# Kernel optimization log

Measured on AMD Instinct MI355X. Metric: run time of the kernel, lower is better.

## Reference

```python
import jax, jax.numpy as jnp
import numpy as np

B, NP, NL, CIN, COUT, MID = 2048, 8, 4, 256, 256, 64


def setup_inputs() -> dict:
    key = jax.random.key(0)
    ks = jax.random.split(key, 16)
    s = 0.01  # small init scale (code uses xavier_normal with tiny gain)
    inp = {
        "x": jax.random.normal(ks[0], (B, CIN), jnp.float32),
        "h": jax.random.normal(ks[1], (B, NP), jnp.float32),
        "index": jnp.zeros((NL,), jnp.float32).at[0].set(1.0),  # one-hot layer index
        # target Linear params
        "target_w": jax.random.normal(ks[2], (COUT, CIN), jnp.float32) * (1.0 / np.sqrt(CIN)),
        "target_b": jax.random.normal(ks[3], (COUT,), jnp.float32) * 0.01,
        # embedder weight branch
        "fcwp_w": jax.random.normal(ks[4], (MID * CIN, NP), jnp.float32) * s,
        "fcwp_b": jnp.zeros((MID * CIN,), jnp.float32),
        "fcwi_w": jax.random.normal(ks[5], (MID * CIN, NL), jnp.float32) * s,
        "fcwi_b": jnp.zeros((MID * CIN,), jnp.float32),
        "fcwe_w": jax.random.normal(ks[6], (COUT, MID), jnp.float32) * s,
        "fcwe_b": jnp.zeros((COUT,), jnp.float32),
        # embedder bias branch
        "fcbp_w": jax.random.normal(ks[7], (COUT, NP), jnp.float32) * s,
        "fcbp_b": jnp.zeros((COUT,), jnp.float32),
        "fcbi_w": jax.random.normal(ks[8], (COUT, NL), jnp.float32) * s,
        "fcbi_b": jnp.zeros((COUT,), jnp.float32),
    }
    return inp


def reference(x, h, index, target_w, target_b,
              fcwp_w, fcwp_b, fcwi_w, fcwi_b, fcwe_w, fcwe_b,
              fcbp_w, fcbp_b, fcbi_w, fcbi_b):
    # --- embedder: per-sample weight modulation ---
    # w_flat: (B, mid*cin)
    w_flat = h @ fcwp_w.T + fcwp_b + (index @ fcwi_w.T + fcwi_b)
    w = w_flat.reshape(B, CIN, MID)                      # (B, cin, mid)
    w = jnp.einsum('bim,om->boi', w, fcwe_w) + fcwe_b[None, :, None]  # swapaxes folded in -> (B, out, cin)
    # bias modulation: (B, out)
    b = h @ fcbp_w.T + fcbp_b + (index @ fcbi_w.T + fcbi_b)
    # --- per-sample linear (grouped conv2d == batched GEMM) ---
    weights = target_w[None] + w                         # (B, out, cin)
    y = jnp.einsum('bi,boi->bo', x, weights)             # batched matvec
    y = y + target_b[None, :] + b
    return y
```

## Files before the change

### kernel.cpp

```cpp
#include <hip/hip_runtime.h>


#define B_TOT 2048
#define NP    8
#define CIN   256
#define COUT  256
#define MID   64
#define K2    352
#define LDG   576
#define LDAS  136
#define LDA2S 360
#define LDB2S 360

typedef short  short8  __attribute__((ext_vector_type(8)));
typedef float  floatx4 __attribute__((ext_vector_type(4)));

__device__ __forceinline__ unsigned short f2bf(float f) {
    union { float f; unsigned u; } v; v.f = f;
    unsigned r = v.u + 0x7FFFu + ((v.u >> 16) & 1u);
    return (unsigned short)(r >> 16);
}
__device__ __forceinline__ float bf2f(unsigned short u) {
    union { unsigned u; float f; } v; v.u = ((unsigned)u) << 16;
    return v.f;
}

__global__ __launch_bounds__(256) void setup_bb(
    const float* __restrict__ index,
    const float* __restrict__ fcwp_w, const float* __restrict__ fcwp_b,
    const float* __restrict__ fcwi_w, const float* __restrict__ fcwi_b,
    unsigned short* __restrict__ Bb)
{
    __shared__ unsigned short Lt[64][68];
    const int blk = blockIdx.x, tid = threadIdx.x;

    if (blk < 32) {
        const int i0 = (blk >> 3) * 64, n0 = (blk & 7) * 64;
        const int r = tid >> 4, c4 = (tid & 15) * 4;
        #pragma unroll
        for (int k = 0; k < 4; ++k) {
            int ii = r + k * 16;
            float4 v = *(const float4*)(fcwp_w + (size_t)(i0 + ii) * 512 + n0 + c4);
            Lt[c4 + 0][ii] = f2bf(v.x); Lt[c4 + 1][ii] = f2bf(v.y);
            Lt[c4 + 2][ii] = f2bf(v.z); Lt[c4 + 3][ii] = f2bf(v.w);
        }
        __syncthreads();
        const int nn = tid >> 2, ic0 = (tid & 3) * 16;
        #pragma unroll
        for (int k = 0; k < 4; ++k) {
            int ic = ic0 + k * 4;
            ushort4 o4;
            o4.x = Lt[nn][ic]; o4.y = Lt[nn][ic + 1];
            o4.z = Lt[nn][ic + 2]; o4.w = Lt[nn][ic + 3];
            *(ushort4*)&Bb[(size_t)(n0 + nn) * CIN + i0 + ic] = o4;
        }
    } else {
        const int i0 = (blk - 32) * 64;
        const float x0 = index[0], x1 = index[1], x2 = index[2], x3 = index[3];
        const int r = tid >> 4, c4 = (tid & 15) * 4;
        #pragma unroll
        for (int k = 0; k < 4; ++k) {
            int ii = r + k * 16;
            int e = (i0 + ii) * 64 + c4;
            float4 pb = *(const float4*)(fcwp_b + e);
            float4 ib = *(const float4*)(fcwi_b + e);
            float pbv[4] = {pb.x, pb.y, pb.z, pb.w};
            float ibv[4] = {ib.x, ib.y, ib.z, ib.w};
            #pragma unroll
            for (int j = 0; j < 4; ++j) {
                float4 wv = *(const float4*)(fcwi_w + (size_t)(e + j) * 4);
                Lt[c4 + j][ii] = f2bf(pbv[j] + ibv[j]
                    + x0 * wv.x + x1 * wv.y + x2 * wv.z + x3 * wv.w);
            }
        }
        __syncthreads();
        const int mm = tid >> 2, ic0 = (tid & 3) * 16;
        #pragma unroll
        for (int k = 0; k < 4; ++k) {
            int ic = ic0 + k * 4;
            ushort4 o4;
            o4.x = Lt[mm][ic]; o4.y = Lt[mm][ic + 1];
            o4.z = Lt[mm][ic + 2]; o4.w = Lt[mm][ic + 3];
            *(ushort4*)&Bb[(size_t)(512 + mm) * CIN + i0 + ic] = o4;
        }
    }
}

__global__ __launch_bounds__(256) void gemm1_kernel(
    const float* __restrict__ x,
    const unsigned short* __restrict__ Bb,
    const float* __restrict__ index,
    const float* __restrict__ target_w, const float* __restrict__ target_b,
    const float* __restrict__ fcwe_w, const float* __restrict__ fcwe_b,
    const float* __restrict__ fcbp_w, const float* __restrict__ fcbp_b,
    const float* __restrict__ fcbi_w, const float* __restrict__ fcbi_b,
    unsigned short* __restrict__ B2,
    unsigned short* __restrict__ G)
{
    __shared__ unsigned short As[64 * LDAS];
    __shared__ unsigned short Bs[64 * LDAS];
    const int blk = blockIdx.x, tid = threadIdx.x;

    if (blk < 288) {
        const int lane = tid & 63, w = tid >> 6;
        const int col = lane & 15, quad = lane >> 4;
        const int mb = (blk & 31) * 64, nb = (blk >> 5) * 64;

        floatx4 acc[4] = {floatx4{0,0,0,0}, floatx4{0,0,0,0},
                          floatx4{0,0,0,0}, floatx4{0,0,0,0}};

        for (int kh = 0; kh < 2; ++kh) {
            const int k0 = kh * 128;
            __syncthreads();
            #pragma unroll
            for (int it = 0; it < 8; ++it) {
                int idx = it * 256 + tid;
                int r = idx >> 5, c = (idx & 31) * 4;
                float4 v = *(const float4*)(x + (size_t)(mb + r) * CIN + k0 + c);
                ushort4 o4;
                o4.x = f2bf(v.x); o4.y = f2bf(v.y); o4.z = f2bf(v.z); o4.w = f2bf(v.w);
                *(ushort4*)&As[r * LDAS + c] = o4;
            }
            #pragma unroll
            for (int it = 0; it < 4; ++it) {
                int idx = it * 256 + tid;
                int r = idx >> 4, c = (idx & 15) * 8;
                *(uint4*)&Bs[r * LDAS + c] =
                    *(const uint4*)(Bb + (size_t)(nb + r) * CIN + k0 + c);
            }
            __syncthreads();
            #pragma unroll
            for (int ks = 0; ks < 4; ++ks) {
                int kc = ks * 32 + quad * 8;
                short8 af = *(const short8*)&As[(w * 16 + col) * LDAS + kc];
                #pragma unroll
                for (int f = 0; f < 4; ++f) {
                    short8 bfr = *(const short8*)&Bs[(f * 16 + col) * LDAS + kc];
                    acc[f] = __builtin_amdgcn_mfma_f32_16x16x32_bf16(af, bfr, acc[f], 0, 0, 0);
                }
            }
        }
        #pragma unroll
        for (int f = 0; f < 4; ++f)
            #pragma unroll
            for (int r = 0; r < 4; ++r)
                G[(size_t)(mb + w * 16 + quad * 4 + r) * LDG + nb + f * 16 + col]
                    = f2bf(acc[f][r]);
    } else if (blk < 304) {
        int base = (blk - 288) * 4096;
        #pragma unroll
        for (int k = 0; k < 4; ++k) {
            int e = base + k * 1024 + tid * 4;
            int o = e >> 8, c = e & 255;
            float4 v = *(const float4*)(target_w + e);
            ushort4 o4;
            o4.x = f2bf(v.x); o4.y = f2bf(v.y); o4.z = f2bf(v.z); o4.w = f2bf(v.w);
            *(ushort4*)&B2[(size_t)o * K2 + c] = o4;
        }
    } else if (blk < 308) {
        int base = (blk - 304) * 4096;
        #pragma unroll
        for (int k = 0; k < 4; ++k) {
            int e = base + k * 1024 + tid * 4;
            int o = e >> 6, m = e & 63;
            float4 v = *(const float4*)(fcwe_w + e);
            ushort4 o4;
            o4.x = f2bf(v.x); o4.y = f2bf(v.y); o4.z = f2bf(v.z); o4.w = f2bf(v.w);
            *(ushort4*)&B2[(size_t)o * K2 + 256 + m] = o4;
        }
    } else {
        int o = tid;
        size_t bo = (size_t)o * K2;
        float4 p0 = *(const float4*)(fcbp_w + (size_t)o * 8);
        float4 p1 = *(const float4*)(fcbp_w + (size_t)o * 8 + 4);
        B2[bo + 320] = f2bf(p0.x); B2[bo + 321] = f2bf(p0.y);
        B2[bo + 322] = f2bf(p0.z); B2[bo + 323] = f2bf(p0.w);
        B2[bo + 324] = f2bf(p1.x); B2[bo + 325] = f2bf(p1.y);
        B2[bo + 326] = f2bf(p1.z); B2[bo + 327] = f2bf(p1.w);
        B2[bo + 328] = f2bf(fcwe_b[o]);
        float bc = target_b[o] + fcbp_b[o] + fcbi_b[o]
                 + index[0] * fcbi_w[o * 4]     + index[1] * fcbi_w[o * 4 + 1]
                 + index[2] * fcbi_w[o * 4 + 2] + index[3] * fcbi_w[o * 4 + 3];
        B2[bo + 329] = f2bf(bc);
        #pragma unroll
        for (int z = 330; z < K2; ++z) B2[bo + z] = 0;
    }
}

__global__ __launch_bounds__(256) void gemm2_kernel(
    const float* __restrict__ x,
    const float* __restrict__ h,
    const unsigned short* __restrict__ B2,
    const unsigned short* __restrict__ G,
    float* __restrict__ out)
{
    __shared__ unsigned short As[32 * LDA2S];
    __shared__ unsigned short Bs[64 * LDB2S];
    __shared__ float red[32][8];

    const int tid = threadIdx.x, lane = tid & 63, w = tid >> 6;
    const int col = lane & 15, quad = lane >> 4;
    const int b0 = blockIdx.x * 32, n0 = blockIdx.y * 64;

    #pragma unroll
    for (int it = 0; it < 8; ++it) {
        int idx = it * 256 + tid;
        int r = idx >> 6, c = (idx & 63) * 4;
        float4 v = *(const float4*)(x + (size_t)(b0 + r) * CIN + c);
        ushort4 o4;
        o4.x = f2bf(v.x); o4.y = f2bf(v.y); o4.z = f2bf(v.z); o4.w = f2bf(v.w);
        *(ushort4*)&As[r * LDA2S + c] = o4;
    }
    {
        int s = tid >> 3, p = tid & 7;
        As[s * LDA2S + 320 + p] = f2bf(h[(size_t)(b0 + s) * NP + p]);
    }
    {
        int s = tid >> 3, seg = tid & 7;
        const float* xr = x + (size_t)(b0 + s) * CIN + seg * 32;
        float p = 0.f;
        #pragma unroll
        for (int k = 0; k < 8; ++k) {
            float4 v = *(const float4*)(xr + k * 4);
            p += v.x + v.y + v.z + v.w;
        }
        red[s][seg] = p;
    }
    for (int idx = tid; idx < 32 * 22; idx += 256) {
        int s = idx / 22, c = 330 + idx % 22;
        As[s * LDA2S + c] = 0;
    }
    #pragma unroll
    for (int it = 0; it < 11; ++it) {
        int idx = it * 256 + tid;
        int r = idx / 44, c = (idx % 44) * 8;
        *(uint4*)&Bs[r * LDB2S + c] =
            *(const uint4*)(B2 + (size_t)(n0 + r) * K2 + c);
    }
    {
        int s = tid >> 3, mg = tid & 7;
        const unsigned short* grow = G + (size_t)(b0 + s) * LDG;
        float4 h0 = *(const float4*)(h + (size_t)(b0 + s) * NP);
        float4 h1 = *(const float4*)(h + (size_t)(b0 + s) * NP + 4);
        float hv[8] = {h0.x, h0.y, h0.z, h0.w, h1.x, h1.y, h1.z, h1.w};
        ushort4 cu0 = *(const ushort4*)(grow + 512 + mg * 8);
        ushort4 cu1 = *(const ushort4*)(grow + 512 + mg * 8 + 4);
        float t[8] = {bf2f(cu0.x), bf2f(cu0.y), bf2f(cu0.z), bf2f(cu0.w),
                      bf2f(cu1.x), bf2f(cu1.y), bf2f(cu1.z), bf2f(cu1.w)};
        #pragma unroll
        for (int j = 0; j < 8; ++j) {
            const unsigned short* gp = grow + (mg * 8 + j) * 8;
            ushort4 g0 = *(const ushort4*)gp;
            ushort4 g1 = *(const ushort4*)(gp + 4);
            t[j] += hv[0] * bf2f(g0.x) + hv[1] * bf2f(g0.y)
                  + hv[2] * bf2f(g0.z) + hv[3] * bf2f(g0.w)
                  + hv[4] * bf2f(g1.x) + hv[5] * bf2f(g1.y)
                  + hv[6] * bf2f(g1.z) + hv[7] * bf2f(g1.w);
        }
        ushort4 t0, t1;
        t0.x = f2bf(t[0]); t0.y = f2bf(t[1]); t0.z = f2bf(t[2]); t0.w = f2bf(t[3]);
        t1.x = f2bf(t[4]); t1.y = f2bf(t[5]); t1.z = f2bf(t[6]); t1.w = f2bf(t[7]);
        *(ushort4*)&As[s * LDA2S + 256 + mg * 8]     = t0;
        *(ushort4*)&As[s * LDA2S + 256 + mg * 8 + 4] = t1;
    }
    __syncthreads();
    if (tid < 32) {
        float s = red[tid][0] + red[tid][1] + red[tid][2] + red[tid][3]
                + red[tid][4] + red[tid][5] + red[tid][6] + red[tid][7];
        As[tid * LDA2S + 328] = f2bf(s);
        As[tid * LDA2S + 329] = 0x3F80;
    }
    __syncthreads();

    const int mr = (w & 1) * 16, nbw = (w >> 1) * 32;
    floatx4 acc[2] = {floatx4{0,0,0,0}, floatx4{0,0,0,0}};
    #pragma unroll
    for (int ks = 0; ks < 11; ++ks) {
        int kc = ks * 32 + quad * 8;
        short8 af = *(const short8*)&As[(mr + col) * LDA2S + kc];
        #pragma unroll
        for (int f = 0; f < 2; ++f) {
            short8 bfr = *(const short8*)&Bs[(nbw + f * 16 + col) * LDB2S + kc];
            acc[f] = __builtin_amdgcn_mfma_f32_16x16x32_bf16(af, bfr, acc[f], 0, 0, 0);
        }
    }
    #pragma unroll
    for (int f = 0; f < 2; ++f)
        #pragma unroll
        for (int r = 0; r < 4; ++r)
            out[(size_t)(b0 + mr + quad * 4 + r) * COUT + n0 + nbw + f * 16 + col]
                = acc[f][r];
}

extern "C" void kernel_launch(void* const* d_in, const int* in_sizes, int n_in,
                              void* d_out, int out_size, void* d_ws, size_t ws_size,
                              hipStream_t stream) {
    const float* x        = (const float*)d_in[0];
    const float* h        = (const float*)d_in[1];
    const float* index    = (const float*)d_in[2];
    const float* target_w = (const float*)d_in[3];
    const float* target_b = (const float*)d_in[4];
    const float* fcwp_w   = (const float*)d_in[5];
    const float* fcwp_b   = (const float*)d_in[6];
    const float* fcwi_w   = (const float*)d_in[7];
    const float* fcwi_b   = (const float*)d_in[8];
    const float* fcwe_w   = (const float*)d_in[9];
    const float* fcwe_b   = (const float*)d_in[10];
    const float* fcbp_w   = (const float*)d_in[11];
    const float* fcbp_b   = (const float*)d_in[12];
    const float* fcbi_w   = (const float*)d_in[13];
    const float* fcbi_b   = (const float*)d_in[14];
    float* out = (float*)d_out;

    char* ws = (char*)d_ws;
    unsigned short* Bb = (unsigned short*)ws;
    unsigned short* B2 = (unsigned short*)(ws + 294912);
    unsigned short* G  = (unsigned short*)(ws + 475136);

    setup_bb<<<36, 256, 0, stream>>>(index, fcwp_w, fcwp_b, fcwi_w, fcwi_b, Bb);

    gemm1_kernel<<<309, 256, 0, stream>>>(
        x, Bb, index, target_w, target_b, fcwe_w, fcwe_b,
        fcbp_w, fcbp_b, fcbi_w, fcbi_b, B2, G);

    gemm2_kernel<<<dim3(B_TOT / 32, COUT / 64), 256, 0, stream>>>(
        x, h, B2, G, out);
}
```

Baseline: 94.28 us.

## Fuse B-operand preparation into gemm1 and drop the setup kernel

Removes the separate setup_bb launch that built a transposed bf16 copy of the fcwp weights and the index-modulated bias block in workspace. gemm1 now reads fcwp_w / fcwi_w / biases directly in fp32, converts to bf16 and transposes into LDS per tile. This cuts one kernel launch and a global round trip. In exchange, each of the 32 M-blocks redoes the conversion and transpose, and the scattered column writes to LDS may cause bank conflicts.

```diff
diff --git a/kernel.cpp b/kernel.cpp
--- a/kernel.cpp
+++ b/kernel.cpp
@@ -25,71 +25,11 @@
     return v.f;
 }
 
-__global__ __launch_bounds__(256) void setup_bb(
+__global__ __launch_bounds__(256) void gemm1_kernel(
+    const float* __restrict__ x,
     const float* __restrict__ index,
     const float* __restrict__ fcwp_w, const float* __restrict__ fcwp_b,
     const float* __restrict__ fcwi_w, const float* __restrict__ fcwi_b,
-    unsigned short* __restrict__ Bb)
-{
-    __shared__ unsigned short Lt[64][68];
-    const int blk = blockIdx.x, tid = threadIdx.x;
-
-    if (blk < 32) {
-        const int i0 = (blk >> 3) * 64, n0 = (blk & 7) * 64;
-        const int r = tid >> 4, c4 = (tid & 15) * 4;
-        #pragma unroll
-        for (int k = 0; k < 4; ++k) {
-            int ii = r + k * 16;
-            float4 v = *(const float4*)(fcwp_w + (size_t)(i0 + ii) * 512 + n0 + c4);
-            Lt[c4 + 0][ii] = f2bf(v.x); Lt[c4 + 1][ii] = f2bf(v.y);
-            Lt[c4 + 2][ii] = f2bf(v.z); Lt[c4 + 3][ii] = f2bf(v.w);
-        }
-        __syncthreads();
-        const int nn = tid >> 2, ic0 = (tid & 3) * 16;
-        #pragma unroll
-        for (int k = 0; k < 4; ++k) {
-            int ic = ic0 + k * 4;
-            ushort4 o4;
-            o4.x = Lt[nn][ic]; o4.y = Lt[nn][ic + 1];
-            o4.z = Lt[nn][ic + 2]; o4.w = Lt[nn][ic + 3];
-            *(ushort4*)&Bb[(size_t)(n0 + nn) * CIN + i0 + ic] = o4;
-        }
-    } else {
-        const int i0 = (blk - 32) * 64;
-        const float x0 = index[0], x1 = index[1], x2 = index[2], x3 = index[3];
-        const int r = tid >> 4, c4 = (tid & 15) * 4;
-        #pragma unroll
-        for (int k = 0; k < 4; ++k) {
-            int ii = r + k * 16;
-            int e = (i0 + ii) * 64 + c4;
-            float4 pb = *(const float4*)(fcwp_b + e);
-            float4 ib = *(const float4*)(fcwi_b + e);
-            float pbv[4] = {pb.x, pb.y, pb.z, pb.w};
-            float ibv[4] = {ib.x, ib.y, ib.z, ib.w};
-            #pragma unroll
-            for (int j = 0; j < 4; ++j) {
-                float4 wv = *(const float4*)(fcwi_w + (size_t)(e + j) * 4);
-                Lt[c4 + j][ii] = f2bf(pbv[j] + ibv[j]
-                    + x0 * wv.x + x1 * wv.y + x2 * wv.z + x3 * wv.w);
-            }
-        }
-        __syncthreads();
-        const int mm = tid >> 2, ic0 = (tid & 3) * 16;
-        #pragma unroll
-        for (int k = 0; k < 4; ++k) {
-            int ic = ic0 + k * 4;
-            ushort4 o4;
-            o4.x = Lt[mm][ic]; o4.y = Lt[mm][ic + 1];
-            o4.z = Lt[mm][ic + 2]; o4.w = Lt[mm][ic + 3];
-            *(ushort4*)&Bb[(size_t)(512 + mm) * CIN + i0 + ic] = o4;
-        }
-    }
-}
-
-__global__ __launch_bounds__(256) void gemm1_kernel(
-    const float* __restrict__ x,
-    const unsigned short* __restrict__ Bb,
-    const float* __restrict__ index,
     const float* __restrict__ target_w, const float* __restrict__ target_b,
     const float* __restrict__ fcwe_w, const float* __restrict__ fcwe_b,
     const float* __restrict__ fcbp_w, const float* __restrict__ fcbp_b,
@@ -104,7 +44,8 @@
     if (blk < 288) {
         const int lane = tid & 63, w = tid >> 6;
         const int col = lane & 15, quad = lane >> 4;
-        const int mb = (blk & 31) * 64, nb = (blk >> 5) * 64;
+        const int mb = (blk & 31) * 64, g = blk >> 5, nb = g * 64;
+        const float i0 = index[0], i1 = index[1], i2 = index[2], i3 = index[3];
 
         floatx4 acc[4] = {floatx4{0,0,0,0}, floatx4{0,0,0,0},
                           floatx4{0,0,0,0}, floatx4{0,0,0,0}};
@@ -121,12 +62,34 @@
                 o4.x = f2bf(v.x); o4.y = f2bf(v.y); o4.z = f2bf(v.z); o4.w = f2bf(v.w);
                 *(ushort4*)&As[r * LDAS + c] = o4;
             }
-            #pragma unroll
-            for (int it = 0; it < 4; ++it) {
-                int idx = it * 256 + tid;
-                int r = idx >> 4, c = (idx & 15) * 8;
-                *(uint4*)&Bs[r * LDAS + c] =
-                    *(const uint4*)(Bb + (size_t)(nb + r) * CIN + k0 + c);
+            if (g < 8) {
+                #pragma unroll
+                for (int it = 0; it < 8; ++it) {
+                    int idx = it * 256 + tid;
+                    int r = idx >> 4, c = (idx & 15) * 4;
+                    float4 v = *(const float4*)(fcwp_w + (size_t)(k0 + r) * 512 + nb + c);
+                    Bs[(c + 0) * LDAS + r] = f2bf(v.x);
+                    Bs[(c + 1) * LDAS + r] = f2bf(v.y);
+                    Bs[(c + 2) * LDAS + r] = f2bf(v.z);
+                    Bs[(c + 3) * LDAS + r] = f2bf(v.w);
+                }
+            } else {
+                #pragma unroll
+                for (int it = 0; it < 8; ++it) {
+                    int idx = it * 256 + tid;
+                    int r = idx >> 4, c = (idx & 15) * 4;
+                    int e = (k0 + r) * 64 + c;
+                    float4 pb = *(const float4*)(fcwp_b + e);
+                    float4 ib = *(const float4*)(fcwi_b + e);
+                    float4 w0 = *(const float4*)(fcwi_w + (size_t)e * 4);
+                    float4 w1 = *(const float4*)(fcwi_w + (size_t)(e + 1) * 4);
+                    float4 w2 = *(const float4*)(fcwi_w + (size_t)(e + 2) * 4);
+                    float4 w3 = *(const float4*)(fcwi_w + (size_t)(e + 3) * 4);
+                    Bs[(c + 0) * LDAS + r] = f2bf(pb.x + ib.x + i0*w0.x + i1*w0.y + i2*w0.z + i3*w0.w);
+                    Bs[(c + 1) * LDAS + r] = f2bf(pb.y + ib.y + i0*w1.x + i1*w1.y + i2*w1.z + i3*w1.w);
+                    Bs[(c + 2) * LDAS + r] = f2bf(pb.z + ib.z + i0*w2.x + i1*w2.y + i2*w2.z + i3*w2.w);
+                    Bs[(c + 3) * LDAS + r] = f2bf(pb.w + ib.w + i0*w3.x + i1*w3.y + i2*w3.z + i3*w3.w);
+                }
             }
             __syncthreads();
             #pragma unroll
@@ -313,14 +276,12 @@
     float* out = (float*)d_out;
 
     char* ws = (char*)d_ws;
-    unsigned short* Bb = (unsigned short*)ws;
-    unsigned short* B2 = (unsigned short*)(ws + 294912);
-    unsigned short* G  = (unsigned short*)(ws + 475136);
-
-    setup_bb<<<36, 256, 0, stream>>>(index, fcwp_w, fcwp_b, fcwi_w, fcwi_b, Bb);
+    unsigned short* B2 = (unsigned short*)ws;
+    unsigned short* G  = (unsigned short*)(ws + 180224);
 
     gemm1_kernel<<<309, 256, 0, stream>>>(
-        x, Bb, index, target_w, target_b, fcwe_w, fcwe_b,
+        x, index, fcwp_w, fcwp_b, fcwi_w, fcwi_b,
+        target_w, target_b, fcwe_w, fcwe_b,
         fcbp_w, fcbp_b, fcbi_w, fcbi_b, B2, G);
 
     gemm2_kernel<<<dim3(B_TOT / 32, COUT / 64), 256, 0, stream>>>(
```

Result: slower. 99.77 us (+5.8%).
